# Kernel tuning notes

Hardware: AMD Instinct MI355X
Metric: run time of the kernel (lower is better)

Reference implementation:

```python
import jax, jax.numpy as jnp
import numpy as np

MAX_POS = 8192
SOFT_CAP = 5.0


def rms_norm(x, scale, eps=1e-6):
    # RMSBatchNorm approximated as RMS normalization over channels with learned scale
    return x * jax.lax.rsqrt(jnp.mean(x * x, axis=-1, keepdims=True) + eps) * scale


def layer_norm(x, scale, offset, eps=1e-5):
    mean = jnp.mean(x, axis=-1, keepdims=True)
    var = jnp.mean(jnp.square(x - mean), axis=-1, keepdims=True)
    return (x - mean) * jax.lax.rsqrt(var + eps) * scale + offset


def apply_rope(x, max_position=MAX_POS):
    # x: [B, S, H, C]
    B, S, H, C = x.shape
    positions = jnp.arange(S, dtype=x.dtype).reshape(1, S)
    num_freq = C // 2
    inv_freq = (1.0 / (jnp.arange(num_freq) + jnp.geomspace(1, max_position - num_freq + 1, num_freq))).astype(x.dtype)
    theta = jnp.einsum('bs,f->bsf', positions, inv_freq)
    theta = jnp.repeat(theta, 2, axis=-1)[..., None, :]  # [1, S, 1, C]
    x_rotated = jnp.stack([-x[..., 1::2], x[..., ::2]], axis=-1).reshape(x.shape)
    return x * jnp.cos(theta) + x_rotated * jnp.sin(theta)


def setup_inputs() -> dict:
    key = jax.random.key(0)
    ks = jax.random.split(key, 16)
    B, S, D = 2, 2048, 1536
    H, CQK, CV = 8, 128, 192
    inp = {
        'x': jax.random.normal(ks[0], (B, S, D), jnp.float32),
        'attention_bias': jax.random.normal(ks[1], (B, H, S, S), jnp.float32),
        'rms_in_scale': jnp.ones((D,), jnp.float32),
        'wq': jax.random.normal(ks[2], (D, H * CQK), jnp.float32) / np.sqrt(D),
        'wk': jax.random.normal(ks[3], (D, CQK), jnp.float32) / np.sqrt(D),
        'wv': jax.random.normal(ks[4], (D, CV), jnp.float32) / np.sqrt(D),
        'q_scale': jnp.ones((CQK,), jnp.float32),
        'q_offset': jnp.zeros((CQK,), jnp.float32),
        'k_scale': jnp.ones((CQK,), jnp.float32),
        'k_offset': jnp.zeros((CQK,), jnp.float32),
        'v_scale': jnp.ones((CV,), jnp.float32),
        'v_offset': jnp.zeros((CV,), jnp.float32),
        'wo': jax.random.normal(ks[5], (H * CV, D), jnp.float32) / np.sqrt(H * CV),
        'bo': jnp.zeros((D,), jnp.float32),
        'rms_out_scale': jnp.ones((D,), jnp.float32),
    }
    return inp


def reference(x, attention_bias, rms_in_scale, wq, wk, wv, q_scale, q_offset,
              k_scale, k_offset, v_scale, v_offset, wo, bo, rms_out_scale):
    B, S, D = x.shape
    H, CQK, CV = 8, 128, 192
    h = rms_norm(x, rms_in_scale)
    q = layer_norm((h @ wq).reshape(B, S, H, CQK), q_scale, q_offset)
    k = layer_norm((h @ wk).reshape(B, S, 1, CQK), k_scale, k_offset)
    v = layer_norm((h @ wv).reshape(B, S, 1, CV), v_scale, v_offset)
    q = apply_rope(q)
    k = apply_rope(k)
    # MQA logits: single shared K head
    logits = jnp.einsum('bshc,bSc->bhsS', q, k[:, :, 0], preferred_element_type=jnp.float32)
    logits = logits / np.sqrt(128.0)
    logits = (logits + attention_bias).astype(jnp.float32)
    logits = jnp.tanh(logits / SOFT_CAP) * SOFT_CAP
    weights = jax.nn.softmax(logits, axis=-1)
    y = jnp.einsum('bhsS,bSc->bshc', weights, v[:, :, 0]).astype(q.dtype)
    y = y.reshape(B, S, H * CV) @ wo + bo
    return rms_norm(y, rms_out_scale)
```

## Files before the change

kernel.cpp:

```cpp
#include <hip/hip_runtime.h>
#include <hip/hip_bf16.h>

typedef unsigned short u16;
typedef short bf16x8 __attribute__((ext_vector_type(8)));
typedef float f32x4 __attribute__((ext_vector_type(4)));

#define NB 2
#define NS 2048
#define ND 1536
#define NH 8
#define NCQK 128
#define NCV 192
#define NBS 4096
#define NPAD 1408

__device__ __forceinline__ float bf2f(u16 u) {
  unsigned v = ((unsigned)u) << 16;
  return __builtin_bit_cast(float, v);
}
__device__ __forceinline__ u16 f2bf(float f) {
  unsigned u = __builtin_bit_cast(unsigned, f);
  u += 0x7fffu + ((u >> 16) & 1u);
  return (u16)(u >> 16);
}
__device__ __forceinline__ void glds16(const u16* g, u16* l) {
  __builtin_amdgcn_global_load_lds(
      (const __attribute__((address_space(1))) void*)g,
      (__attribute__((address_space(3))) void*)l, 16, 0, 0);
}
__device__ __forceinline__ f32x4 mfma16(bf16x8 a, bf16x8 b, f32x4 c) {
  return __builtin_amdgcn_mfma_f32_16x16x32_bf16(a, b, c, 0, 0, 0);
}

__global__ void transpose_k(const float* __restrict__ in, u16* __restrict__ out,
                            int K, int N) {
  __shared__ float t[64][65];
  const int n0 = blockIdx.x * 64, k0 = blockIdx.y * 64;
  const int tid = threadIdx.x;
  const int rl = tid >> 4, cl = (tid & 15) * 4;
  for (int p = 0; p < 4; p++) {
    int k = rl + p * 16;
    float4 v = *(const float4*)(in + (size_t)(k0 + k) * N + n0 + cl);
    t[k][cl] = v.x; t[k][cl + 1] = v.y; t[k][cl + 2] = v.z; t[k][cl + 3] = v.w;
  }
  __syncthreads();
  const int rn = tid >> 3, ck = (tid & 7) * 8;
  for (int p = 0; p < 2; p++) {
    int n = rn + p * 32;
    u16 tmp[8];
    for (int j = 0; j < 8; j++) tmp[j] = f2bf(t[ck + j][n]);
    *(uint4*)(out + (size_t)(n0 + n) * K + k0 + ck) = *(uint4*)tmp;
  }
}

__global__ void rmsnorm_in_k(const float* __restrict__ x, const float* __restrict__ scale,
                             u16* __restrict__ h) {
  __shared__ float sbuf[4];
  const int row = blockIdx.x, tid = threadIdx.x;
  const float* xr = x + (size_t)row * ND;
  float v[6]; float ss = 0.f;
  for (int i = 0; i < 6; i++) { v[i] = xr[tid + i * 256]; ss += v[i] * v[i]; }
  for (int o = 32; o; o >>= 1) ss += __shfl_xor(ss, o);
  if ((tid & 63) == 0) sbuf[tid >> 6] = ss;
  __syncthreads();
  ss = sbuf[0] + sbuf[1] + sbuf[2] + sbuf[3];
  const float inv = rsqrtf(ss * (1.f / ND) + 1e-6f);
  u16* hr = h + (size_t)row * ND;
  for (int i = 0; i < 6; i++) {
    int c = tid + i * 256;
    hr[c] = f2bf(v[i] * inv * scale[c]);
  }
}

template <bool F32OUT>
__global__ __launch_bounds__(256, 2)
void gemm_nt(const u16* __restrict__ A, const u16* __restrict__ Bt,
             float* __restrict__ Cf, u16* __restrict__ Cb, int M, int N, int K) {
  __shared__ __align__(16) u16 As[128 * 64];
  __shared__ __align__(16) u16 Bs[128 * 64];
  const int tid = threadIdx.x;
  const int wave = tid >> 6, lane = tid & 63, quad = lane >> 4, l16 = lane & 15;
  const int m0 = blockIdx.y * 128, n0 = blockIdx.x * 128;
  const int mrb = (wave & 1) * 4, nrb = (wave >> 1) * 4;
  f32x4 acc[4][4] = {};
  for (int k0 = 0; k0 < K; k0 += 64) {
    if (k0) __syncthreads();
    for (int i = 0; i < 4; i++) {
      int g = wave * 4 + i;
      int rb = g >> 1, kh = g & 1;
      int row = rb * 16 + l16, kc = kh * 4 + quad;
      glds16(A + (size_t)(m0 + row) * K + k0 + kc * 8, &As[(rb * 8 + kh * 4) * 128]);
      glds16(Bt + (size_t)(n0 + row) * K + k0 + kc * 8, &Bs[(rb * 8 + kh * 4) * 128]);
    }
    __syncthreads();
    for (int kk = 0; kk < 2; kk++) {
      bf16x8 af[4], bfr[4];
      for (int f = 0; f < 4; f++)
        af[f] = *(const bf16x8*)&As[(((mrb + f) * 8 + kk * 4 + quad) * 16 + l16) * 8];
      for (int f = 0; f < 4; f++)
        bfr[f] = *(const bf16x8*)&Bs[(((nrb + f) * 8 + kk * 4 + quad) * 16 + l16) * 8];
      for (int mf = 0; mf < 4; mf++)
        for (int nf = 0; nf < 4; nf++)
          acc[mf][nf] = mfma16(af[mf], bfr[nf], acc[mf][nf]);
    }
  }
  for (int mf = 0; mf < 4; mf++)
    for (int nf = 0; nf < 4; nf++)
      for (int r = 0; r < 4; r++) {
        int m = m0 + (wave & 1) * 64 + mf * 16 + quad * 4 + r;
        int n = n0 + (wave >> 1) * 64 + nf * 16 + l16;
        if (F32OUT) Cf[(size_t)m * N + n] = acc[mf][nf][r];
        else        Cb[(size_t)m * N + n] = f2bf(acc[mf][nf][r]);
      }
}

__global__ void ln_rope_k(const float* __restrict__ qkv,
                          const float* __restrict__ qs, const float* __restrict__ qo,
                          const float* __restrict__ ks, const float* __restrict__ ko,
                          const float* __restrict__ vs, const float* __restrict__ vo,
                          u16* __restrict__ Qg, u16* __restrict__ Kg, u16* __restrict__ Vg) {
  const int row = blockIdx.x;
  const int b = row >> 11, s = row & (NS - 1);
  const int wave = threadIdx.x >> 6, lane = threadIdx.x & 63;
  const float* base = qkv + (size_t)row * NPAD;
  const float gsp = __expf(logf(8129.f) * ((float)lane * (1.f / 63.f)));
  const float invf = 1.f / ((float)lane + gsp);
  float sn, cs;
  sincosf((float)s * invf, &sn, &cs);

  for (int hh = 0; hh < 2; hh++) {
    const int h = wave * 2 + hh;
    const float* p = base + h * NCQK;
    float x0 = p[lane * 2], x1 = p[lane * 2 + 1];
    float s1 = x0 + x1, s2 = x0 * x0 + x1 * x1;
    for (int o = 32; o; o >>= 1) { s1 += __shfl_xor(s1, o); s2 += __shfl_xor(s2, o); }
    float mean = s1 * (1.f / NCQK);
    float inv = rsqrtf(s2 * (1.f / NCQK) - mean * mean + 1e-5f);
    float y0 = (x0 - mean) * inv * qs[lane * 2] + qo[lane * 2];
    float y1 = (x1 - mean) * inv * qs[lane * 2 + 1] + qo[lane * 2 + 1];
    u16* dst = Qg + (size_t)row * (NH * NCQK) + h * NCQK + lane * 2;
    dst[0] = f2bf(y0 * cs - y1 * sn);
    dst[1] = f2bf(y1 * cs + y0 * sn);
  }
  if (wave == 0) {
    const float* p = base + NH * NCQK;
    float x0 = p[lane * 2], x1 = p[lane * 2 + 1];
    float s1 = x0 + x1, s2 = x0 * x0 + x1 * x1;
    for (int o = 32; o; o >>= 1) { s1 += __shfl_xor(s1, o); s2 += __shfl_xor(s2, o); }
    float mean = s1 * (1.f / NCQK);
    float inv = rsqrtf(s2 * (1.f / NCQK) - mean * mean + 1e-5f);
    float y0 = (x0 - mean) * inv * ks[lane * 2] + ko[lane * 2];
    float y1 = (x1 - mean) * inv * ks[lane * 2 + 1] + ko[lane * 2 + 1];
    u16* dst = Kg + (size_t)row * NCQK + lane * 2;
    dst[0] = f2bf(y0 * cs - y1 * sn);
    dst[1] = f2bf(y1 * cs + y0 * sn);
  }
  if (wave == 1) {
    const float* p = base + NH * NCQK + NCQK;
    float x[3]; float s1 = 0.f, s2 = 0.f;
    for (int i = 0; i < 3; i++) { x[i] = p[lane + i * 64]; s1 += x[i]; s2 += x[i] * x[i]; }
    for (int o = 32; o; o >>= 1) { s1 += __shfl_xor(s1, o); s2 += __shfl_xor(s2, o); }
    float mean = s1 * (1.f / NCV);
    float inv = rsqrtf(s2 * (1.f / NCV) - mean * mean + 1e-5f);
    for (int i = 0; i < 3; i++) {
      int c = lane + i * 64;
      float y = (x[i] - mean) * inv * vs[c] + vo[c];
      Vg[(size_t)(b * NCV + c) * NS + s] = f2bf(y);
    }
  }
}

__global__ __launch_bounds__(256, 2)
void attn_k(const u16* __restrict__ Qg, const u16* __restrict__ Kg,
            const u16* __restrict__ Vg, const float* __restrict__ bias,
            u16* __restrict__ Y) {
  __shared__ __align__(16) u16 Qs[64 * 128];
  __shared__ __align__(16) u16 Ks[64 * 128];
  __shared__ __align__(16) u16 Vs[192 * 64];
  __shared__ __align__(16) u16 Ps[64 * 64];
  const int tid = threadIdx.x;
  const int wave = tid >> 6, lane = tid & 63, quad = lane >> 4, l16 = lane & 15;
  const int s0 = blockIdx.x * 64;
  const int h = blockIdx.y, b = blockIdx.z;

  const u16* Kbase = Kg + (size_t)(b * NS) * NCQK;
  const u16* Vbase = Vg + (size_t)(b * NCV) * NS;
  const float* brow = bias + ((size_t)(b * NH + h) * NS + s0 + wave * 16) * NS;

  for (int i = 0; i < 4; i++) {
    glds16(Qg + ((size_t)((b * NS + s0 + wave * 16 + l16) * NH + h)) * NCQK + (i * 4 + quad) * 8,
           &Qs[(wave * 16 + i * 4) * 128]);
    glds16(Kbase + (size_t)(wave * 16 + l16) * NCQK + (i * 4 + quad) * 8,
           &Ks[(wave * 16 + i * 4) * 128]);
  }
  for (int i = 0; i < 6; i++) {
    int g = wave * 6 + i;
    int cb = g >> 1, kh = g & 1;
    glds16(Vbase + (size_t)(cb * 16 + l16) * NS + (kh * 4 + quad) * 8,
           &Vs[(cb * 8 + kh * 4) * 128]);
  }
  float breg[16];
  for (int nb = 0; nb < 4; nb++)
    for (int r = 0; r < 4; r++)
      breg[nb * 4 + r] = brow[(size_t)(quad * 4 + r) * NS + nb * 16 + l16];
  __syncthreads();

  bf16x8 qa[4];
  for (int kk = 0; kk < 4; kk++)
    qa[kk] = *(const bf16x8*)&Qs[((wave * 16 + kk * 4 + quad) * 16 + l16) * 8];

  f32x4 oacc[12] = {};
  float lsum[4] = {0.f, 0.f, 0.f, 0.f};

  for (int kt = 0; kt < NS / 64; kt++) {
    f32x4 sacc[4] = {};
    for (int kk = 0; kk < 4; kk++)
      for (int nb = 0; nb < 4; nb++) {
        bf16x8 kf = *(const bf16x8*)&Ks[((nb * 16 + kk * 4 + quad) * 16 + l16) * 8];
        sacc[nb] = mfma16(qa[kk], kf, sacc[nb]);
      }

    for (int nb = 0; nb < 4; nb++) {
      const int key_l = nb * 16 + l16;
      for (int r = 0; r < 4; r++) {
        const int qrow = quad * 4 + r;
        float sv = sacc[nb][r] * 0.08838834764831845f + breg[nb * 4 + r];
        float e2 = __expf(sv * 0.4f);
        float cap = 5.f - 10.f / (e2 + 1.f);
        u16 pb = f2bf(__expf(cap));
        lsum[r] += bf2f(pb);
        Ps[((wave * 8 + (key_l >> 3)) * 16 + qrow) * 8 + (key_l & 7)] = pb;
      }
    }

    for (int kk = 0; kk < 2; kk++) {
      bf16x8 pa = *(const bf16x8*)&Ps[((wave * 8 + kk * 4 + quad) * 16 + l16) * 8];
      for (int nb = 0; nb < 12; nb++) {
        bf16x8 vf = *(const bf16x8*)&Vs[((nb * 8 + kk * 4 + quad) * 16 + l16) * 8];
        oacc[nb] = mfma16(pa, vf, oacc[nb]);
      }
    }

    if (kt + 1 < NS / 64) {
      const int key0 = (kt + 1) * 64;
      for (int nb = 0; nb < 4; nb++)
        for (int r = 0; r < 4; r++)
          breg[nb * 4 + r] = brow[(size_t)(quad * 4 + r) * NS + key0 + nb * 16 + l16];
      __syncthreads();
      for (int i = 0; i < 4; i++)
        glds16(Kbase + (size_t)(key0 + wave * 16 + l16) * NCQK + (i * 4 + quad) * 8,
               &Ks[(wave * 16 + i * 4) * 128]);
      for (int i = 0; i < 6; i++) {
        int g = wave * 6 + i;
        int cb = g >> 1, kh = g & 1;
        glds16(Vbase + (size_t)(cb * 16 + l16) * NS + key0 + (kh * 4 + quad) * 8,
               &Vs[(cb * 8 + kh * 4) * 128]);
      }
      __syncthreads();
    }
  }

  for (int r = 0; r < 4; r++)
    for (int o = 1; o < 16; o <<= 1) lsum[r] += __shfl_xor(lsum[r], o);
  for (int r = 0; r < 4; r++) {
    const float inv = 1.f / lsum[r];
    const int m = s0 + wave * 16 + quad * 4 + r;
    u16* yr = Y + (size_t)(b * NS + m) * ND + h * NCV;
    for (int nb = 0; nb < 12; nb++) yr[nb * 16 + l16] = f2bf(oacc[nb][r] * inv);
  }
}

__global__ void final_k(const u16* __restrict__ yo, const float* __restrict__ bo,
                        const float* __restrict__ scale, float* __restrict__ out) {
  __shared__ float sbuf[4];
  const int row = blockIdx.x, tid = threadIdx.x;
  const u16* yr = yo + (size_t)row * ND;
  float v[6]; float ss = 0.f;
  for (int i = 0; i < 6; i++) {
    int c = tid + i * 256;
    v[i] = bf2f(yr[c]) + bo[c];
    ss += v[i] * v[i];
  }
  for (int o = 32; o; o >>= 1) ss += __shfl_xor(ss, o);
  if ((tid & 63) == 0) sbuf[tid >> 6] = ss;
  __syncthreads();
  ss = sbuf[0] + sbuf[1] + sbuf[2] + sbuf[3];
  const float inv = rsqrtf(ss * (1.f / ND) + 1e-6f);
  float* orow = out + (size_t)row * ND;
  for (int i = 0; i < 6; i++) {
    int c = tid + i * 256;
    orow[c] = v[i] * inv * scale[c];
  }
}

extern "C" void kernel_launch(void* const* d_in, const int* in_sizes, int n_in,
                              void* d_out, int out_size, void* d_ws, size_t ws_size,
                              hipStream_t stream) {
  const float* x    = (const float*)d_in[0];
  const float* bias = (const float*)d_in[1];
  const float* rin  = (const float*)d_in[2];
  const float* wq   = (const float*)d_in[3];
  const float* wk   = (const float*)d_in[4];
  const float* wv   = (const float*)d_in[5];
  const float* qsc  = (const float*)d_in[6];
  const float* qof  = (const float*)d_in[7];
  const float* ksc  = (const float*)d_in[8];
  const float* kof  = (const float*)d_in[9];
  const float* vsc  = (const float*)d_in[10];
  const float* vof  = (const float*)d_in[11];
  const float* wo   = (const float*)d_in[12];
  const float* bo   = (const float*)d_in[13];
  const float* rout = (const float*)d_in[14];

  char* ws = (char*)d_ws;
  size_t off = 0;
  auto alloc = [&](size_t bytes) -> void* {
    void* p = ws + off;
    off += (bytes + 255) & ~(size_t)255;
    return p;
  };
  u16*   h    = (u16*)alloc((size_t)NBS * ND * 2);
  u16*   wtq  = (u16*)alloc((size_t)NPAD * ND * 2);
  u16*   wto  = (u16*)alloc((size_t)ND * ND * 2);
  float* qkv  = (float*)alloc((size_t)NBS * NPAD * 4);
  u16*   Qb   = (u16*)alloc((size_t)NBS * NH * NCQK * 2);
  u16*   Kb   = (u16*)alloc((size_t)NBS * NCQK * 2);
  u16*   Vtb  = (u16*)alloc((size_t)NB * NCV * NS * 2);
  u16*   Ybf  = (u16*)alloc((size_t)NBS * ND * 2);
  u16*   Yob  = (u16*)alloc((size_t)NBS * ND * 2);

  transpose_k<<<dim3(16, 24), 256, 0, stream>>>(wq, wtq, ND, 1024);
  transpose_k<<<dim3(2, 24), 256, 0, stream>>>(wk, wtq + (size_t)1024 * ND, ND, 128);
  transpose_k<<<dim3(3, 24), 256, 0, stream>>>(wv, wtq + (size_t)1152 * ND, ND, 192);
  transpose_k<<<dim3(24, 24), 256, 0, stream>>>(wo, wto, ND, ND);
  rmsnorm_in_k<<<NBS, 256, 0, stream>>>(x, rin, h);
  gemm_nt<true><<<dim3(NPAD / 128, NBS / 128), 256, 0, stream>>>(h, wtq, qkv, nullptr, NBS, NPAD, ND);
  ln_rope_k<<<NBS, 256, 0, stream>>>(qkv, qsc, qof, ksc, kof, vsc, vof, Qb, Kb, Vtb);
  attn_k<<<dim3(NS / 64, NH, NB), 256, 0, stream>>>(Qb, Kb, Vtb, bias, Ybf);
  gemm_nt<false><<<dim3(ND / 128, NBS / 128), 256, 0, stream>>>(Ybf, wto, nullptr, Yob, NBS, ND, ND);
  final_k<<<NBS, 256, 0, stream>>>(Yob, bo, rout, (float*)d_out);
}
```

Before: 594.1 us.

## Double-buffer K/V tiles with 32-key steps and streamline softcap exp math

Restructures the attention kernel main loop to use 32-key tiles with double-buffered K/V in shared memory. The next tile's global-to-LDS load is issued before computing on the current one, so one barrier per iteration replaces two. Q now loads straight into registers, and P uses a per-wave LDS buffer. The tanh-softcap and exp chain is folded into fused constants using raw v_exp_f32, rcp and a packed bf16 convert, which cuts ALU work but adds loop iterations and more barrier overhead per key.

```diff
diff --git a/kernel.cpp b/kernel.cpp
--- a/kernel.cpp
+++ b/kernel.cpp
@@ -174,90 +174,116 @@
 void attn_k(const u16* __restrict__ Qg, const u16* __restrict__ Kg,
             const u16* __restrict__ Vg, const float* __restrict__ bias,
             u16* __restrict__ Y) {
-  __shared__ __align__(16) u16 Qs[64 * 128];
-  __shared__ __align__(16) u16 Ks[64 * 128];
-  __shared__ __align__(16) u16 Vs[192 * 64];
-  __shared__ __align__(16) u16 Ps[64 * 64];
+  __shared__ __align__(16) u16 Ks[2][32 * 128];
+  __shared__ __align__(16) u16 Vs[2][192 * 32];
+  __shared__ __align__(16) u16 Ps[4][512];
   const int tid = threadIdx.x;
   const int wave = tid >> 6, lane = tid & 63, quad = lane >> 4, l16 = lane & 15;
   const int s0 = blockIdx.x * 64;
   const int h = blockIdx.y, b = blockIdx.z;
 
+  const float C1 = 0.0510069742f;
+  const float C2 = 0.5770780163f;
+  const float C3 = -14.4269504089f;
+  const float C4 = 7.2134752044f;
+
+  bf16x8 qa[4];
+  {
+    const u16* qr = Qg + ((size_t)((b * NS + s0 + wave * 16 + l16) * NH + h)) * NCQK;
+#pragma unroll
+    for (int kk = 0; kk < 4; kk++)
+      qa[kk] = *(const bf16x8*)(qr + (kk * 4 + quad) * 8);
+  }
+
   const u16* Kbase = Kg + (size_t)(b * NS) * NCQK;
   const u16* Vbase = Vg + (size_t)(b * NCV) * NS;
-  const float* brow = bias + ((size_t)(b * NH + h) * NS + s0 + wave * 16) * NS;
-
-  for (int i = 0; i < 4; i++) {
-    glds16(Qg + ((size_t)((b * NS + s0 + wave * 16 + l16) * NH + h)) * NCQK + (i * 4 + quad) * 8,
-           &Qs[(wave * 16 + i * 4) * 128]);
-    glds16(Kbase + (size_t)(wave * 16 + l16) * NCQK + (i * 4 + quad) * 8,
-           &Ks[(wave * 16 + i * 4) * 128]);
-  }
-  for (int i = 0; i < 6; i++) {
-    int g = wave * 6 + i;
-    int cb = g >> 1, kh = g & 1;
-    glds16(Vbase + (size_t)(cb * 16 + l16) * NS + (kh * 4 + quad) * 8,
-           &Vs[(cb * 8 + kh * 4) * 128]);
-  }
-  float breg[16];
-  for (int nb = 0; nb < 4; nb++)
+  const float* bp = bias + ((size_t)(b * NH + h) * NS + s0 + wave * 16 + quad * 4) * NS + l16;
+
+  const u16* ksrc[2];
+#pragma unroll
+  for (int i = 0; i < 2; i++) {
+    int g = wave * 2 + i, kb = g >> 2, kh = g & 3;
+    ksrc[i] = Kbase + (size_t)(kb * 16 + l16) * NCQK + (kh * 4 + quad) * 8;
+  }
+  const u16* vsrc[3];
+#pragma unroll
+  for (int i = 0; i < 3; i++) {
+    int g = wave * 3 + i;
+    vsrc[i] = Vbase + (size_t)(g * 16 + l16) * NS + quad * 8;
+  }
+
+  auto stage = [&](int buf, int key0) {
+#pragma unroll
+    for (int i = 0; i < 2; i++) {
+      int g = wave * 2 + i;
+      glds16(ksrc[i] + (size_t)key0 * NCQK, &Ks[buf][g * 512]);
+    }
+#pragma unroll
+    for (int i = 0; i < 3; i++) {
+      int g = wave * 3 + i;
+      glds16(vsrc[i] + key0, &Vs[buf][g * 512]);
+    }
+  };
+
+  float breg[8];
+  auto loadB = [&](int key0) {
+#pragma unroll
     for (int r = 0; r < 4; r++)
-      breg[nb * 4 + r] = brow[(size_t)(quad * 4 + r) * NS + nb * 16 + l16];
-  __syncthreads();
-
-  bf16x8 qa[4];
-  for (int kk = 0; kk < 4; kk++)
-    qa[kk] = *(const bf16x8*)&Qs[((wave * 16 + kk * 4 + quad) * 16 + l16) * 8];
+#pragma unroll
+      for (int nb = 0; nb < 2; nb++)
+        breg[r * 2 + nb] = bp[(size_t)r * NS + key0 + nb * 16];
+  };
+
+  const int rbase = quad * 128 + l16 * 8;
+  const int pwbase = (l16 >> 3) * 128 + quad * 32 + (l16 & 7);
 
   f32x4 oacc[12] = {};
   float lsum[4] = {0.f, 0.f, 0.f, 0.f};
 
-  for (int kt = 0; kt < NS / 64; kt++) {
-    f32x4 sacc[4] = {};
+  stage(0, 0);
+  loadB(0);
+  __syncthreads();
+
+  for (int kt = 0; kt < NS / 32; kt++) {
+    const int cur = kt & 1;
+    if (kt + 1 < NS / 32) stage(cur ^ 1, (kt + 1) * 32);
+
+    f32x4 sacc[2] = {};
+#pragma unroll
     for (int kk = 0; kk < 4; kk++)
-      for (int nb = 0; nb < 4; nb++) {
-        bf16x8 kf = *(const bf16x8*)&Ks[((nb * 16 + kk * 4 + quad) * 16 + l16) * 8];
+#pragma unroll
+      for (int nb = 0; nb < 2; nb++) {
+        bf16x8 kf = *(const bf16x8*)&Ks[cur][(nb * 4 + kk) * 512 + rbase];
         sacc[nb] = mfma16(qa[kk], kf, sacc[nb]);
       }
 
-    for (int nb = 0; nb < 4; nb++) {
-      const int key_l = nb * 16 + l16;
+#pragma unroll
+    for (int nb = 0; nb < 2; nb++)
+#pragma unroll
       for (int r = 0; r < 4; r++) {
-        const int qrow = quad * 4 + r;
-        float sv = sacc[nb][r] * 0.08838834764831845f + breg[nb * 4 + r];
-        float e2 = __expf(sv * 0.4f);
-        float cap = 5.f - 10.f / (e2 + 1.f);
-        u16 pb = f2bf(__expf(cap));
-        lsum[r] += bf2f(pb);
-        Ps[((wave * 8 + (key_l >> 3)) * 16 + qrow) * 8 + (key_l & 7)] = pb;
+        float a = fmaf(sacc[nb][r], C1, breg[r * 2 + nb] * C2);
+        float e2;
+        asm("v_exp_f32 %0, %1" : "=v"(e2) : "v"(a));
+        float u = __builtin_amdgcn_rcpf(e2 + 1.f);
+        float a2 = fmaf(u, C3, C4);
+        float p;
+        asm("v_exp_f32 %0, %1" : "=v"(p) : "v"(a2));
+        unsigned pk;
+        asm("v_cvt_pk_bf16_f32 %0, %1, %2" : "=v"(pk) : "v"(p), "v"(p));
+        lsum[r] += __builtin_bit_cast(float, pk << 16);
+        Ps[wave][pwbase + nb * 256 + r * 8] = (u16)pk;
       }
-    }
-
-    for (int kk = 0; kk < 2; kk++) {
-      bf16x8 pa = *(const bf16x8*)&Ps[((wave * 8 + kk * 4 + quad) * 16 + l16) * 8];
-      for (int nb = 0; nb < 12; nb++) {
-        bf16x8 vf = *(const bf16x8*)&Vs[((nb * 8 + kk * 4 + quad) * 16 + l16) * 8];
-        oacc[nb] = mfma16(pa, vf, oacc[nb]);
-      }
-    }
-
-    if (kt + 1 < NS / 64) {
-      const int key0 = (kt + 1) * 64;
-      for (int nb = 0; nb < 4; nb++)
-        for (int r = 0; r < 4; r++)
-          breg[nb * 4 + r] = brow[(size_t)(quad * 4 + r) * NS + key0 + nb * 16 + l16];
-      __syncthreads();
-      for (int i = 0; i < 4; i++)
-        glds16(Kbase + (size_t)(key0 + wave * 16 + l16) * NCQK + (i * 4 + quad) * 8,
-               &Ks[(wave * 16 + i * 4) * 128]);
-      for (int i = 0; i < 6; i++) {
-        int g = wave * 6 + i;
-        int cb = g >> 1, kh = g & 1;
-        glds16(Vbase + (size_t)(cb * 16 + l16) * NS + key0 + (kh * 4 + quad) * 8,
-               &Vs[(cb * 8 + kh * 4) * 128]);
-      }
-      __syncthreads();
-    }
+
+    if (kt + 1 < NS / 32) loadB((kt + 1) * 32);
+
+    bf16x8 pa = *(const bf16x8*)&Ps[wave][rbase];
+#pragma unroll
+    for (int nb = 0; nb < 12; nb++) {
+      bf16x8 vf = *(const bf16x8*)&Vs[cur][nb * 512 + rbase];
+      oacc[nb] = mfma16(pa, vf, oacc[nb]);
+    }
+
+    if (kt + 1 < NS / 32) __syncthreads();
   }
 
   for (int r = 0; r < 4; r++)
```

After: 624.9 us. +5.2%, slower.

## Tune attention kernel occupancy, drop Q LDS staging, streamline softcap math

Applied to the files above, without the earlier changes.

Q fragments are now loaded straight from global memory into registers instead of going through shared memory, which frees LDS and lets the launch bound ask for 3 blocks per CU. The tanh-softcap-exp chain is rewritten with folded constants, raw v_exp_f32, rcp and a packed bf16 convert. The bias prefetch for the next tile is moved ahead of the PV MFMAs so its latency is hidden, and s_setprio wraps the MFMA sections. The risks are register spills under the tighter bound and a small accuracy change from the approximate exp and rcp.

```diff
diff --git a/kernel.cpp b/kernel.cpp
--- a/kernel.cpp
+++ b/kernel.cpp
@@ -170,11 +170,10 @@
   }
 }
 
-__global__ __launch_bounds__(256, 2)
+__global__ __launch_bounds__(256, 3)
 void attn_k(const u16* __restrict__ Qg, const u16* __restrict__ Kg,
             const u16* __restrict__ Vg, const float* __restrict__ bias,
             u16* __restrict__ Y) {
-  __shared__ __align__(16) u16 Qs[64 * 128];
   __shared__ __align__(16) u16 Ks[64 * 128];
   __shared__ __align__(16) u16 Vs[192 * 64];
   __shared__ __align__(16) u16 Ps[64 * 64];
@@ -183,76 +182,107 @@
   const int s0 = blockIdx.x * 64;
   const int h = blockIdx.y, b = blockIdx.z;
 
+  const float C1 = 0.0510069742f;
+  const float C2 = 0.5770780163f;
+  const float C3 = -14.4269504089f;
+  const float C4 = 7.2134752044f;
+
+  bf16x8 qa[4];
+  {
+    const u16* qr = Qg + ((size_t)((b * NS + s0 + wave * 16 + l16) * NH + h)) * NCQK;
+#pragma unroll
+    for (int kk = 0; kk < 4; kk++)
+      qa[kk] = *(const bf16x8*)(qr + (kk * 4 + quad) * 8);
+  }
+
   const u16* Kbase = Kg + (size_t)(b * NS) * NCQK;
   const u16* Vbase = Vg + (size_t)(b * NCV) * NS;
   const float* brow = bias + ((size_t)(b * NH + h) * NS + s0 + wave * 16) * NS;
 
-  for (int i = 0; i < 4; i++) {
-    glds16(Qg + ((size_t)((b * NS + s0 + wave * 16 + l16) * NH + h)) * NCQK + (i * 4 + quad) * 8,
-           &Qs[(wave * 16 + i * 4) * 128]);
+#pragma unroll
+  for (int i = 0; i < 4; i++)
     glds16(Kbase + (size_t)(wave * 16 + l16) * NCQK + (i * 4 + quad) * 8,
            &Ks[(wave * 16 + i * 4) * 128]);
-  }
+#pragma unroll
   for (int i = 0; i < 6; i++) {
-    int g = wave * 6 + i;
-    int cb = g >> 1, kh = g & 1;
+    int g = wave * 6 + i, cb = g >> 1, kh = g & 1;
     glds16(Vbase + (size_t)(cb * 16 + l16) * NS + (kh * 4 + quad) * 8,
            &Vs[(cb * 8 + kh * 4) * 128]);
   }
   float breg[16];
+#pragma unroll
   for (int nb = 0; nb < 4; nb++)
+#pragma unroll
     for (int r = 0; r < 4; r++)
       breg[nb * 4 + r] = brow[(size_t)(quad * 4 + r) * NS + nb * 16 + l16];
   __syncthreads();
 
-  bf16x8 qa[4];
-  for (int kk = 0; kk < 4; kk++)
-    qa[kk] = *(const bf16x8*)&Qs[((wave * 16 + kk * 4 + quad) * 16 + l16) * 8];
-
   f32x4 oacc[12] = {};
   float lsum[4] = {0.f, 0.f, 0.f, 0.f};
 
   for (int kt = 0; kt < NS / 64; kt++) {
     f32x4 sacc[4] = {};
+    __builtin_amdgcn_s_setprio(1);
+#pragma unroll
     for (int kk = 0; kk < 4; kk++)
+#pragma unroll
       for (int nb = 0; nb < 4; nb++) {
         bf16x8 kf = *(const bf16x8*)&Ks[((nb * 16 + kk * 4 + quad) * 16 + l16) * 8];
         sacc[nb] = mfma16(qa[kk], kf, sacc[nb]);
       }
-
+    __builtin_amdgcn_s_setprio(0);
+
+#pragma unroll
     for (int nb = 0; nb < 4; nb++) {
       const int key_l = nb * 16 + l16;
+#pragma unroll
       for (int r = 0; r < 4; r++) {
         const int qrow = quad * 4 + r;
-        float sv = sacc[nb][r] * 0.08838834764831845f + breg[nb * 4 + r];
-        float e2 = __expf(sv * 0.4f);
-        float cap = 5.f - 10.f / (e2 + 1.f);
-        u16 pb = f2bf(__expf(cap));
-        lsum[r] += bf2f(pb);
-        Ps[((wave * 8 + (key_l >> 3)) * 16 + qrow) * 8 + (key_l & 7)] = pb;
-      }
-    }
-
+        float a = fmaf(sacc[nb][r], C1, breg[nb * 4 + r] * C2);
+        float e2;
+        asm("v_exp_f32 %0, %1" : "=v"(e2) : "v"(a));
+        float u = __builtin_amdgcn_rcpf(e2 + 1.f);
+        float a2 = fmaf(u, C3, C4);
+        float p;
+        asm("v_exp_f32 %0, %1" : "=v"(p) : "v"(a2));
+        unsigned pk;
+        asm("v_cvt_pk_bf16_f32 %0, %1, %2" : "=v"(pk) : "v"(p), "v"(p));
+        lsum[r] += __builtin_bit_cast(float, pk << 16);
+        Ps[((wave * 8 + (key_l >> 3)) * 16 + qrow) * 8 + (key_l & 7)] = (u16)pk;
+      }
+    }
+
+    if (kt + 1 < NS / 64) {
+      const int key0 = (kt + 1) * 64;
+#pragma unroll
+      for (int nb = 0; nb < 4; nb++)
+#pragma unroll
+        for (int r = 0; r < 4; r++)
+          breg[nb * 4 + r] = brow[(size_t)(quad * 4 + r) * NS + key0 + nb * 16 + l16];
+    }
+
+    __builtin_amdgcn_s_setprio(1);
+#pragma unroll
     for (int kk = 0; kk < 2; kk++) {
       bf16x8 pa = *(const bf16x8*)&Ps[((wave * 8 + kk * 4 + quad) * 16 + l16) * 8];
+#pragma unroll
       for (int nb = 0; nb < 12; nb++) {
         bf16x8 vf = *(const bf16x8*)&Vs[((nb * 8 + kk * 4 + quad) * 16 + l16) * 8];
         oacc[nb] = mfma16(pa, vf, oacc[nb]);
       }
     }
+    __builtin_amdgcn_s_setprio(0);
 
     if (kt + 1 < NS / 64) {
       const int key0 = (kt + 1) * 64;
-      for (int nb = 0; nb < 4; nb++)
-        for (int r = 0; r < 4; r++)
-          breg[nb * 4 + r] = brow[(size_t)(quad * 4 + r) * NS + key0 + nb * 16 + l16];
       __syncthreads();
+#pragma unroll
       for (int i = 0; i < 4; i++)
         glds16(Kbase + (size_t)(key0 + wave * 16 + l16) * NCQK + (i * 4 + quad) * 8,
                &Ks[(wave * 16 + i * 4) * 128]);
+#pragma unroll
       for (int i = 0; i < 6; i++) {
-        int g = wave * 6 + i;
-        int cb = g >> 1, kh = g & 1;
+        int g = wave * 6 + i, cb = g >> 1, kh = g & 1;
         glds16(Vbase + (size_t)(cb * 16 + l16) * NS + key0 + (kh * 4 + quad) * 8,
                &Vs[(cb * 8 + kh * 4) * 128]);
       }
```

Measured after the change: 590.1 us. Within noise of the previous version (-0.7%).
